# Kernel tuning notes

Hardware: AMD Instinct MI355X
Metric: run time of the kernel (lower is better)

## Reference

```python
import jax, jax.numpy as jnp
import numpy as np

STRIDE = (1, 1)
PADDING = ((1, 1), (1, 1))


def setup_inputs() -> dict:
    key = jax.random.key(0)
    kx, kw, kb = jax.random.split(key, 3)
    x = jax.random.normal(kx, (32, 128, 56, 56), dtype=jnp.float32)
    weight = jax.random.normal(kw, (256, 128, 3, 3), dtype=jnp.float32)  # (O, I, kh, kw)
    bias = jax.random.normal(kb, (256,), dtype=jnp.float32)
    return {"x": x, "weight": weight, "bias": bias}


def reference(x, weight, bias):
    # Faithful dense 2D convolution (cross-correlation, as in the torch module),
    # NCHW input, OIHW weight, stride 1, padding 1.
    out = jax.lax.conv_general_dilated(
        x, weight,
        window_strides=STRIDE,
        padding=PADDING,
        dimension_numbers=("NCHW", "OIHW", "NCHW"),
    )
    return out + bias[None, :, None, None]
```

## Files before the change

kernel.cpp:

```cpp
#include <hip/hip_runtime.h>

#define C_IN   128
#define H_IN   56
#define W_IN   56
#define HW     3136
#define CHW    401408
#define O_OUT  256
#define OHW    802816

#define BM 256
#define BN 128
#define LDSW 64
#define LDK 72
#define XTP 132

typedef __bf16 bf16x8 __attribute__((ext_vector_type(8)));
typedef float  f32x4  __attribute__((ext_vector_type(4)));
typedef unsigned short ushort_t;
typedef ushort_t ushort8 __attribute__((ext_vector_type(8)));

__device__ __forceinline__ ushort_t f2bf(float f) {
    union { float f; unsigned u; } v; v.f = f;
    unsigned r = (v.u + 0x7fffu + ((v.u >> 16) & 1u)) >> 16;
    return (ushort_t)r;
}

__global__ void wt_kernel(const float* __restrict__ w, ushort_t* __restrict__ wbf) {
    int idx = blockIdx.x * 256 + threadIdx.x;
    if (idx >= 9 * 256 * 128) return;
    int pos = idx >> 15;
    int rem = idx & 32767;
    int o   = rem >> 7;
    int c   = rem & 127;
    wbf[idx] = f2bf(w[o * 1152 + c * 9 + pos]);
}

__global__ __launch_bounds__(256)
void xt_kernel(const float* __restrict__ x, ushort_t* __restrict__ xb) {
    __shared__ ushort_t T[64 * XTP];
    const int t  = threadIdx.x;
    const int tb = blockIdx.x;
    const int n   = tb / 49;
    const int hw0 = (tb - n * 49) * 64;
    const float* src = x + (long)n * CHW + hw0;

    #pragma unroll
    for (int i = 0; i < 8; ++i) {
        const int g  = i * 256 + t;
        const int c  = g >> 4;
        const int p4 = g & 15;
        f32x4 v = *(const f32x4*)(src + (long)c * HW + p4 * 4);
        #pragma unroll
        for (int j = 0; j < 4; ++j)
            T[(p4 * 4 + j) * XTP + c] = f2bf(v[j]);
    }
    __syncthreads();

    ushort_t* dst = xb + ((long)n * HW + hw0) * 128;
    #pragma unroll
    for (int s = 0; s < 4; ++s) {
        const int idx = s * 256 + t;
        const int pix = idx >> 4;
        const int grp = idx & 15;
        ushort8 v = *(const ushort8*)(&T[pix * XTP + grp * 8]);
        *(ushort8*)(dst + pix * 128 + grp * 8) = v;
    }
}

__global__ __launch_bounds__(512, 4)
void conv2_kernel(const ushort_t* __restrict__ xb, const ushort_t* __restrict__ wbf,
                  const float* __restrict__ bias, float* __restrict__ out) {
    __shared__ ushort_t As[BM * LDSW];
    __shared__ ushort_t Bs[BN * LDSW];

    const int tid  = threadIdx.x;
    const int lane = tid & 63;
    const int wave = tid >> 6;
    const int wm   = wave >> 1;
    const int wn   = wave & 1;
    const int l15  = lane & 15;
    const int quad = lane >> 4;

    const int pix_base = blockIdx.x * BN;

    const int bpx = tid >> 2;
    const int bg0 = (tid & 3) * 2;
    const int p   = pix_base + bpx;
    const int n_img = p / HW;
    const int hw    = p - n_img * HW;
    const int h     = hw / W_IN;
    const int w_    = hw - h * W_IN;

    const int ao = tid >> 3;
    const int ag = tid & 7;

    f32x4 acc[4][4];
    #pragma unroll
    for (int t = 0; t < 4; ++t)
        #pragma unroll
        for (int u = 0; u < 4; ++u)
            acc[t][u] = f32x4{0.f, 0.f, 0.f, 0.f};

    for (int pos = 0; pos < 9; ++pos) {
        const int dh = pos / 3 - 1;
        const int dw = pos - (pos / 3) * 3 - 1;
        const int ih = h + dh;
        const int iw = w_ + dw;
        const bool valid = ((unsigned)ih < (unsigned)H_IN) && ((unsigned)iw < (unsigned)W_IN);
        const ushort_t* bsrc = xb + (long)(p + dh * W_IN + dw) * 128;

        #pragma unroll
        for (int half = 0; half < 2; ++half) {
            const int c0 = half * 64;

            {
                const ushort_t* wsrc = wbf + pos * 32768 + c0;
                #pragma unroll
                for (int s = 0; s < 4; ++s) {
                    const int o = ao + s * 64;
                    ushort8 v = *(const ushort8*)(wsrc + (o << 7) + ag * 8);
                    *(ushort8*)(&As[o * LDSW + ((ag ^ (o & 7)) * 8)]) = v;
                }
            }
            {
                #pragma unroll
                for (int q = 0; q < 2; ++q) {
                    const int g = bg0 + q;
                    ushort8 v;
                    if (valid) v = *(const ushort8*)(bsrc + c0 + g * 8);
                    else       v = ushort8{0,0,0,0,0,0,0,0};
                    *(ushort8*)(&Bs[bpx * LDSW + ((g ^ (bpx & 7)) * 8)]) = v;
                }
            }
            __syncthreads();

            #pragma unroll
            for (int ks = 0; ks < 2; ++ks) {
                bf16x8 af[4], bfv[4];
                const int k16 = ks * 4 + quad;
                #pragma unroll
                for (int t = 0; t < 4; ++t) {
                    const int row = wm * 64 + t * 16 + l15;
                    af[t] = *(const bf16x8*)(&As[row * LDSW + ((k16 ^ (row & 7)) * 8)]);
                }
                #pragma unroll
                for (int u = 0; u < 4; ++u) {
                    const int col = wn * 64 + u * 16 + l15;
                    bfv[u] = *(const bf16x8*)(&Bs[col * LDSW + ((k16 ^ (col & 7)) * 8)]);
                }
                #pragma unroll
                for (int t = 0; t < 4; ++t)
                    #pragma unroll
                    for (int u = 0; u < 4; ++u)
                        acc[t][u] = __builtin_amdgcn_mfma_f32_16x16x32_bf16(af[t], bfv[u], acc[t][u], 0, 0, 0);
            }
            __syncthreads();
        }
    }

    #pragma unroll
    for (int u = 0; u < 4; ++u) {
        const int col = wn * 64 + u * 16 + l15;
        const int pp  = pix_base + col;
        const int nn  = pp / HW;
        const int hw2 = pp - nn * HW;
        const long obase = (long)nn * OHW + hw2;
        #pragma unroll
        for (int t = 0; t < 4; ++t) {
            const int o_base = wm * 64 + t * 16 + quad * 4;
            #pragma unroll
            for (int r = 0; r < 4; ++r) {
                const int o = o_base + r;
                out[obase + (long)o * HW] = acc[t][u][r] + bias[o];
            }
        }
    }
}

__global__ __launch_bounds__(512, 4)
void conv_kernel(const float* __restrict__ x, const ushort_t* __restrict__ wbf,
                 const float* __restrict__ bias, float* __restrict__ out) {
    __shared__ ushort_t As[BM * LDK];
    __shared__ ushort_t Bs[BN * LDK];

    const int tid  = threadIdx.x;
    const int lane = tid & 63;
    const int wave = tid >> 6;
    const int wm   = wave >> 1;
    const int wn   = wave & 1;
    const int l15  = lane & 15;
    const int quad = lane >> 4;

    const int pix_base = blockIdx.x * BN;
    const int px  = tid & 127;
    const int cg0 = tid >> 7;
    const int p   = pix_base + px;
    const int n_img = p / HW;
    const int hw    = p - n_img * HW;
    const int h     = hw / W_IN;
    const int w_    = hw - h * W_IN;
    const float* ximg = x + (long)n_img * CHW;

    f32x4 acc[4][4];
    #pragma unroll
    for (int t = 0; t < 4; ++t)
        #pragma unroll
        for (int u = 0; u < 4; ++u)
            acc[t][u] = f32x4{0.f, 0.f, 0.f, 0.f};

    for (int pos = 0; pos < 9; ++pos) {
        const int dh = pos / 3 - 1;
        const int dw = pos - (pos / 3) * 3 - 1;
        const int ih = h + dh;
        const int iw = w_ + dw;
        const bool valid = ((unsigned)ih < (unsigned)H_IN) && ((unsigned)iw < (unsigned)W_IN);
        const float* xsrc = ximg + ih * W_IN + iw;

        for (int half = 0; half < 2; ++half) {
            const int c0 = half * 64;
            {
                const ushort_t* wsrc = wbf + ((pos * 256) << 7) + c0;
                #pragma unroll
                for (int s = 0; s < 4; ++s) {
                    const int o  = (tid >> 3) + s * 64;
                    const int cg = tid & 7;
                    ushort8 v = *(const ushort8*)(wsrc + (o << 7) + cg * 8);
                    *(ushort8*)(&As[o * LDK + cg * 8]) = v;
                }
            }
            {
                #pragma unroll
                for (int s = 0; s < 2; ++s) {
                    const int cg = cg0 + s * 4;
                    const float* src = xsrc + (long)(c0 + cg * 8) * HW;
                    ushort8 v;
                    #pragma unroll
                    for (int j = 0; j < 8; ++j) {
                        float f = valid ? src[j * HW] : 0.0f;
                        v[j] = f2bf(f);
                    }
                    *(ushort8*)(&Bs[px * LDK + cg * 8]) = v;
                }
            }
            __syncthreads();

            #pragma unroll
            for (int ks = 0; ks < 2; ++ks) {
                bf16x8 af[4], bfv[4];
                #pragma unroll
                for (int t = 0; t < 4; ++t) {
                    const int row = wm * 64 + t * 16 + l15;
                    af[t] = *(const bf16x8*)(&As[row * LDK + ks * 32 + quad * 8]);
                }
                #pragma unroll
                for (int u = 0; u < 4; ++u) {
                    const int col = wn * 64 + u * 16 + l15;
                    bfv[u] = *(const bf16x8*)(&Bs[col * LDK + ks * 32 + quad * 8]);
                }
                #pragma unroll
                for (int t = 0; t < 4; ++t)
                    #pragma unroll
                    for (int u = 0; u < 4; ++u)
                        acc[t][u] = __builtin_amdgcn_mfma_f32_16x16x32_bf16(af[t], bfv[u], acc[t][u], 0, 0, 0);
            }
            __syncthreads();
        }
    }

    #pragma unroll
    for (int u = 0; u < 4; ++u) {
        const int col = wn * 64 + u * 16 + l15;
        const int pp  = pix_base + col;
        const int hw2 = pp - (pp / HW) * HW;
        const long obase = (long)(pp / HW) * OHW + hw2;
        #pragma unroll
        for (int t = 0; t < 4; ++t) {
            const int o_base = wm * 64 + t * 16 + quad * 4;
            #pragma unroll
            for (int r = 0; r < 4; ++r) {
                const int o = o_base + r;
                out[obase + (long)o * HW] = acc[t][u][r] + bias[o];
            }
        }
    }
}

extern "C" void kernel_launch(void* const* d_in, const int* in_sizes, int n_in,
                              void* d_out, int out_size, void* d_ws, size_t ws_size,
                              hipStream_t stream) {
    const float* x    = (const float*)d_in[0];
    const float* w    = (const float*)d_in[1];
    const float* bias = (const float*)d_in[2];
    float* out        = (float*)d_out;

    ushort_t* wbf = (ushort_t*)d_ws;
    ushort_t* xb  = (ushort_t*)((char*)d_ws + 589824);

    const size_t need = 589824u + 25690112u;

    hipLaunchKernelGGL(wt_kernel, dim3(1152), dim3(256), 0, stream, w, wbf);
    if (ws_size >= need) {
        hipLaunchKernelGGL(xt_kernel, dim3(1568), dim3(256), 0, stream, x, xb);
        hipLaunchKernelGGL(conv2_kernel, dim3(100352 / BN), dim3(512), 0, stream,
                           xb, wbf, bias, out);
    } else {
        hipLaunchKernelGGL(conv_kernel, dim3(100352 / BN), dim3(512), 0, stream,
                           x, wbf, bias, out);
    }
}
```

Before: 226.0 us.

## Add padded-NHWC patch conv kernel with LDS-resident input rows and async weight prefetch

Adds a new path: the input is transposed to a zero-padded, swizzled NHWC bf16 layout, and weights are pre-swizzled per 64-channel slice. Each block loads a 6-row input patch (4 output rows plus halo) into LDS once via global_load_lds and reuses it across all 9 filter taps. Weight slices are double-buffered with asynchronous global-to-LDS loads overlapping the MFMA work. This removes repeated per-tap input fetches and bounds checks, at the cost of a larger workspace, heavy LDS use and a larger per-thread accumulator tile (28 MFMA tiles) that may limit occupancy.

```diff
diff --git a/kernel.cpp b/kernel.cpp
--- a/kernel.cpp
+++ b/kernel.cpp
@@ -14,6 +14,10 @@
 #define LDK 72
 #define XTP 132
 
+#define PH 58
+#define PROW 7424
+#define PATCH_PIX 348
+
 typedef __bf16 bf16x8 __attribute__((ext_vector_type(8)));
 typedef float  f32x4  __attribute__((ext_vector_type(4)));
 typedef unsigned short ushort_t;
@@ -24,6 +28,191 @@
     unsigned r = (v.u + 0x7fffu + ((v.u >> 16) & 1u)) >> 16;
     return (ushort_t)r;
 }
+
+typedef const __attribute__((address_space(1))) unsigned int* gas_ptr;
+typedef __attribute__((address_space(3))) unsigned int* las_ptr;
+__device__ __forceinline__ void gl_lds16(const void* g, void* l) {
+    __builtin_amdgcn_global_load_lds((gas_ptr)g, (las_ptr)l, 16, 0, 0);
+}
+
+
+__global__ void wt2_kernel(const float* __restrict__ w, ushort_t* __restrict__ wbf) {
+    int idx = blockIdx.x * 256 + threadIdx.x;
+    if (idx >= 9 * 256 * 128) return;
+    int pos = idx >> 15;
+    int rem = idx & 32767;
+    int o   = rem >> 7;
+    int c   = rem & 127;
+    int s    = pos * 2 + (c >> 6);
+    int slot = ((c >> 3) & 7) ^ (o & 7);
+    wbf[((s * 256 + o) << 6) + (slot << 3) + (c & 7)] = f2bf(w[o * 1152 + c * 9 + pos]);
+}
+
+__global__ __launch_bounds__(256)
+void xt2_kernel(const float* __restrict__ x, ushort_t* __restrict__ xbp) {
+    const int b  = blockIdx.x;
+    const int n  = b / PH;
+    const int hp = b - n * PH;
+    ushort_t* orow = xbp + (size_t)(n * PH + hp) * PROW;
+    const int t = threadIdx.x;
+    ushort8 z = ushort8{0,0,0,0,0,0,0,0};
+
+    if (hp == 0 || hp == 57) {
+        #pragma unroll
+        for (int i = 0; i < 4; ++i) {
+            int u = i * 256 + t;
+            if (u < 928) *(ushort8*)(orow + u * 8) = z;
+        }
+        return;
+    }
+
+    __shared__ ushort_t T[56 * XTP];
+    const int h = hp - 1;
+    const float* src = x + (size_t)n * CHW + h * W_IN;
+    #pragma unroll
+    for (int i = 0; i < 7; ++i) {
+        int g  = i * 256 + t;
+        int c  = g / 14;
+        int f4 = g - c * 14;
+        f32x4 v = *(const f32x4*)(src + (size_t)c * HW + f4 * 4);
+        #pragma unroll
+        for (int j = 0; j < 4; ++j)
+            T[(f4 * 4 + j) * XTP + c] = f2bf(v[j]);
+    }
+    __syncthreads();
+    #pragma unroll
+    for (int i = 0; i < 4; ++i) {
+        int u = i * 256 + t;
+        if (u < 928) {
+            int wp = u >> 4, gg = u & 15;
+            ushort8 v = (wp == 0 || wp == 57) ? z
+                        : *(const ushort8*)(&T[(wp - 1) * XTP + gg * 8]);
+            *(ushort8*)(orow + wp * 128 + ((gg ^ (wp & 7)) << 3)) = v;
+        }
+    }
+}
+
+__global__ __launch_bounds__(512, 2)
+void conv3_kernel(const ushort_t* __restrict__ xbp, const ushort_t* __restrict__ wbf,
+                  const float* __restrict__ bias, float* __restrict__ out) {
+    __shared__ ushort_t patch[PATCH_PIX * 128];
+    __shared__ ushort_t wlds[2][256 * 64];
+
+    const int tid  = threadIdx.x;
+    const int lane = tid & 63;
+    const int wave = tid >> 6;
+    const int wm   = wave >> 1;
+    const int wn   = wave & 1;
+    const int l15  = lane & 15;
+    const int quad = lane >> 4;
+    const int om   = wm * 64;
+
+    const int b  = blockIdx.x;
+    const int n  = b / 14;
+    const int hg = b - n * 14;
+    const int h0 = hg * 4;
+
+    int ppix[7], wlo[7], obo[7];
+    #pragma unroll
+    for (int u = 0; u < 7; ++u) {
+        int p  = wn * 112 + u * 16 + l15;
+        int pr = p / 56;
+        int ww = p - pr * 56;
+        ppix[u] = (pr * PH + ww) * 128;
+        wlo[u]  = ww;
+        obo[u]  = (h0 + pr) * W_IN + ww;
+    }
+
+    f32x4 acc[4][7];
+    #pragma unroll
+    for (int t = 0; t < 4; ++t)
+        #pragma unroll
+        for (int u = 0; u < 7; ++u)
+            acc[t][u] = f32x4{0.f, 0.f, 0.f, 0.f};
+
+    {
+        const char* xs = (const char*)(xbp + (size_t)(n * PH + h0) * PROW);
+        char* pb = (char*)patch;
+        #pragma unroll
+        for (int jj = 0; jj < 11; ++jj) {
+            int j = jj * 8 + wave;
+            if (j < 87) gl_lds16(xs + j * 1024 + lane * 16, pb + j * 1024);
+        }
+        const char* wg = (const char*)wbf;
+        char* wb = (char*)wlds[0];
+        #pragma unroll
+        for (int j2 = 0; j2 < 4; ++j2) {
+            int j = j2 * 8 + wave;
+            gl_lds16(wg + j * 1024 + lane * 16, wb + j * 1024);
+        }
+    }
+    asm volatile("s_waitcnt vmcnt(0)" ::: "memory");
+    __syncthreads();
+
+    int s = 0, cur = 0;
+    for (int kh = 0; kh < 3; ++kh) {
+        #pragma unroll
+        for (int kw = 0; kw < 3; ++kw) {
+            const int poff = (kh * PH + kw) * 128;
+            #pragma unroll
+            for (int half = 0; half < 2; ++half) {
+                const ushort_t* wcur = wlds[cur];
+                if (s < 17) {
+                    const char* wg = (const char*)wbf + (size_t)(s + 1) * 32768;
+                    char* wb = (char*)wlds[cur ^ 1];
+                    #pragma unroll
+                    for (int j2 = 0; j2 < 4; ++j2) {
+                        int j = j2 * 8 + wave;
+                        gl_lds16(wg + j * 1024 + lane * 16, wb + j * 1024);
+                    }
+                }
+                #pragma unroll
+                for (int ks = 0; ks < 2; ++ks) {
+                    const int k8  = ks * 4 + quad;
+                    const int k16 = half * 8 + k8;
+                    bf16x8 af[4], bfv[7];
+                    #pragma unroll
+                    for (int t = 0; t < 4; ++t) {
+                        int o = om + t * 16 + l15;
+                        af[t] = *(const bf16x8*)(wcur + (o << 6) + ((k8 ^ (o & 7)) << 3));
+                    }
+                    #pragma unroll
+                    for (int u = 0; u < 7; ++u) {
+                        int slot = k16 ^ ((wlo[u] + kw) & 7);
+                        bfv[u] = *(const bf16x8*)(patch + ppix[u] + poff + (slot << 3));
+                    }
+                    #pragma unroll
+                    for (int t = 0; t < 4; ++t)
+                        #pragma unroll
+                        for (int u = 0; u < 7; ++u)
+                            acc[t][u] = __builtin_amdgcn_mfma_f32_16x16x32_bf16(
+                                            af[t], bfv[u], acc[t][u], 0, 0, 0);
+                }
+                asm volatile("s_waitcnt vmcnt(0)" ::: "memory");
+                __syncthreads();
+                cur ^= 1; ++s;
+            }
+        }
+    }
+
+    f32x4 bv[4];
+    #pragma unroll
+    for (int t = 0; t < 4; ++t)
+        bv[t] = *(const f32x4*)(bias + om + t * 16 + quad * 4);
+    float* outn = out + (size_t)n * OHW;
+    #pragma unroll
+    for (int u = 0; u < 7; ++u) {
+        float* op = outn + obo[u];
+        #pragma unroll
+        for (int t = 0; t < 4; ++t) {
+            const int o0 = om + t * 16 + quad * 4;
+            #pragma unroll
+            for (int r = 0; r < 4; ++r)
+                op[(size_t)(o0 + r) * HW] = acc[t][u][r] + bv[t][r];
+        }
+    }
+}
+
 
 __global__ void wt_kernel(const float* __restrict__ w, ushort_t* __restrict__ wbf) {
     int idx = blockIdx.x * 256 + threadIdx.x;
@@ -116,8 +305,8 @@
             {
                 const ushort_t* wsrc = wbf + pos * 32768 + c0;
                 #pragma unroll
-                for (int s = 0; s < 4; ++s) {
-                    const int o = ao + s * 64;
+                for (int sj = 0; sj < 4; ++sj) {
+                    const int o = ao + sj * 64;
                     ushort8 v = *(const ushort8*)(wsrc + (o << 7) + ag * 8);
                     *(ushort8*)(&As[o * LDSW + ((ag ^ (o & 7)) * 8)]) = v;
                 }
@@ -221,8 +410,8 @@
             {
                 const ushort_t* wsrc = wbf + ((pos * 256) << 7) + c0;
                 #pragma unroll
-                for (int s = 0; s < 4; ++s) {
-                    const int o  = (tid >> 3) + s * 64;
+                for (int sj = 0; sj < 4; ++sj) {
+                    const int o  = (tid >> 3) + sj * 64;
                     const int cg = tid & 7;
                     ushort8 v = *(const ushort8*)(wsrc + (o << 7) + cg * 8);
                     *(ushort8*)(&As[o * LDK + cg * 8]) = v;
@@ -230,8 +419,8 @@
             }
             {
                 #pragma unroll
-                for (int s = 0; s < 2; ++s) {
-                    const int cg = cg0 + s * 4;
+                for (int sj = 0; sj < 2; ++sj) {
+                    const int cg = cg0 + sj * 4;
                     const float* src = xsrc + (long)(c0 + cg * 8) * HW;
                     ushort8 v;
                     #pragma unroll
@@ -293,17 +482,26 @@
     const float* bias = (const float*)d_in[2];
     float* out        = (float*)d_out;
 
-    ushort_t* wbf = (ushort_t*)d_ws;
-    ushort_t* xb  = (ushort_t*)((char*)d_ws + 589824);
-
-    const size_t need = 589824u + 25690112u;
-
-    hipLaunchKernelGGL(wt_kernel, dim3(1152), dim3(256), 0, stream, w, wbf);
-    if (ws_size >= need) {
+    const size_t NEED_NEW = 589824u + 27557888u;
+    const size_t NEED_OLD = 589824u + 25690112u;
+
+    if (ws_size >= NEED_NEW) {
+        ushort_t* wbf2 = (ushort_t*)d_ws;
+        ushort_t* xbp  = (ushort_t*)((char*)d_ws + 589824);
+        hipLaunchKernelGGL(wt2_kernel, dim3(1152), dim3(256), 0, stream, w, wbf2);
+        hipLaunchKernelGGL(xt2_kernel, dim3(1856), dim3(256), 0, stream, x, xbp);
+        hipLaunchKernelGGL(conv3_kernel, dim3(448), dim3(512), 0, stream,
+                           xbp, wbf2, bias, out);
+    } else if (ws_size >= NEED_OLD) {
+        ushort_t* wbf = (ushort_t*)d_ws;
+        ushort_t* xb  = (ushort_t*)((char*)d_ws + 589824);
+        hipLaunchKernelGGL(wt_kernel, dim3(1152), dim3(256), 0, stream, w, wbf);
         hipLaunchKernelGGL(xt_kernel, dim3(1568), dim3(256), 0, stream, x, xb);
         hipLaunchKernelGGL(conv2_kernel, dim3(100352 / BN), dim3(512), 0, stream,
                            xb, wbf, bias, out);
     } else {
+        ushort_t* wbf = (ushort_t*)d_ws;
+        hipLaunchKernelGGL(wt_kernel, dim3(1152), dim3(256), 0, stream, w, wbf);
         hipLaunchKernelGGL(conv_kernel, dim3(100352 / BN), dim3(512), 0, stream,
                            x, wbf, bias, out);
     }
```

Result: slower. 237.7 us (+5.2%).

## Replace im2col GEMM with halo-patch conv kernel reading weights from global

Applied to the files above, without the earlier changes.

The separate NHWC bf16 transpose pass and the per-tap LDS staging are replaced by a kernel where each block loads a 4x58x128 bf16 halo patch of input once into swizzled LDS. All nine taps then reuse it for two output rows (112 pixels) across 256 output channels. Weights are rearranged into per-tap, per-half slabs and read directly from global/L2 into registers, with no LDS or barriers in the main loop. This removes the extra transpose kernel and repeated input traffic, but relies on L2 for weight bandwidth. It also adds a serial, strided fp32 patch load done by only 232 threads at block start.

```diff
diff --git a/kernel.cpp b/kernel.cpp
--- a/kernel.cpp
+++ b/kernel.cpp
@@ -8,11 +8,7 @@
 #define O_OUT  256
 #define OHW    802816
 
-#define BM 256
-#define BN 128
-#define LDSW 64
 #define LDK 72
-#define XTP 132
 
 typedef __bf16 bf16x8 __attribute__((ext_vector_type(8)));
 typedef float  f32x4  __attribute__((ext_vector_type(4)));
@@ -24,6 +20,130 @@
     unsigned r = (v.u + 0x7fffu + ((v.u >> 16) & 1u)) >> 16;
     return (ushort_t)r;
 }
+
+__global__ void wt3_kernel(const float* __restrict__ w, ushort_t* __restrict__ wbf) {
+    int idx = blockIdx.x * 256 + threadIdx.x;
+    if (idx >= 9 * 256 * 128) return;
+    int pos = idx >> 15;
+    int rem = idx & 32767;
+    int o   = rem >> 7;
+    int c   = rem & 127;
+    int s   = pos * 2 + (c >> 6);
+    wbf[((s * 256 + o) << 6) + (c & 63)] = f2bf(w[o * 1152 + c * 9 + pos]);
+}
+
+__global__ __launch_bounds__(256, 2)
+void conv6_kernel(const float* __restrict__ x, const ushort_t* __restrict__ wbf,
+                  const float* __restrict__ bias, float* __restrict__ out) {
+    __shared__ ushort_t patch[232 * 128];
+
+    const int tid  = threadIdx.x;
+    const int lane = tid & 63;
+    const int wave = tid >> 6;
+    const int l15  = lane & 15;
+    const int quad = lane >> 4;
+    const int om   = wave * 64;
+
+    int b = blockIdx.x;
+    b = (b & 7) * 112 + (b >> 3);
+    const int n  = b / 28;
+    const int h0 = (b - n * 28) * 2;
+
+    if (tid < 232) {
+        const int pr = tid / 58;
+        const int wp = tid - pr * 58;
+        const int ih = h0 - 1 + pr;
+        const int iw = wp - 1;
+        const bool ok = ((unsigned)ih < 56u) && ((unsigned)iw < 56u);
+        const float* xs = x + (size_t)n * CHW + ih * W_IN + iw;
+        ushort_t* dst = patch + tid * 128;
+        const int wkey = wp & 7;
+        #pragma unroll
+        for (int cg = 0; cg < 16; ++cg) {
+            ushort8 v;
+            #pragma unroll
+            for (int j = 0; j < 8; ++j) {
+                float f = 0.0f;
+                if (ok) f = xs[(size_t)(cg * 8 + j) * HW];
+                v[j] = f2bf(f);
+            }
+            *(ushort8*)(dst + (((cg ^ wkey)) << 3)) = v;
+        }
+    }
+    __syncthreads();
+
+    int ppix[7], wk[7], obo[7];
+    #pragma unroll
+    for (int u = 0; u < 7; ++u) {
+        int pix = u * 16 + l15;
+        int pr  = (pix >= 56) ? 1 : 0;
+        int ww  = pix - pr * 56;
+        ppix[u] = (pr * 58 + ww) * 128;
+        wk[u]   = ww;
+        obo[u]  = (h0 + pr) * W_IN + ww;
+    }
+
+    int aoff[4];
+    #pragma unroll
+    for (int t = 0; t < 4; ++t)
+        aoff[t] = ((om + t * 16 + l15) << 6) + (quad << 3);
+
+    f32x4 acc[4][7];
+    #pragma unroll
+    for (int t = 0; t < 4; ++t)
+        #pragma unroll
+        for (int u = 0; u < 7; ++u)
+            acc[t][u] = f32x4{0.f, 0.f, 0.f, 0.f};
+
+    for (int kh = 0; kh < 3; ++kh) {
+        #pragma unroll
+        for (int kw = 0; kw < 3; ++kw) {
+            const int poff = (kh * 58 + kw) * 128;
+            #pragma unroll
+            for (int half = 0; half < 2; ++half) {
+                const int s = (kh * 3 + kw) * 2 + half;
+                const ushort_t* wsp = wbf + (size_t)s * 16384;
+                #pragma unroll
+                for (int ks = 0; ks < 2; ++ks) {
+                    bf16x8 af[4], bfv[7];
+                    #pragma unroll
+                    for (int t = 0; t < 4; ++t)
+                        af[t] = *(const bf16x8*)(wsp + aoff[t] + ks * 32);
+                    const int k16 = half * 8 + ks * 4 + quad;
+                    #pragma unroll
+                    for (int u = 0; u < 7; ++u) {
+                        const int slot = k16 ^ ((wk[u] + kw) & 7);
+                        bfv[u] = *(const bf16x8*)(patch + ppix[u] + poff + (slot << 3));
+                    }
+                    #pragma unroll
+                    for (int t = 0; t < 4; ++t)
+                        #pragma unroll
+                        for (int u = 0; u < 7; ++u)
+                            acc[t][u] = __builtin_amdgcn_mfma_f32_16x16x32_bf16(
+                                            af[t], bfv[u], acc[t][u], 0, 0, 0);
+                }
+            }
+        }
+    }
+
+    f32x4 bv[4];
+    #pragma unroll
+    for (int t = 0; t < 4; ++t)
+        bv[t] = *(const f32x4*)(bias + om + t * 16 + quad * 4);
+    float* outn = out + (size_t)n * OHW;
+    #pragma unroll
+    for (int u = 0; u < 7; ++u) {
+        float* op = outn + obo[u];
+        #pragma unroll
+        for (int t = 0; t < 4; ++t) {
+            const int o0 = om + t * 16 + quad * 4;
+            #pragma unroll
+            for (int r = 0; r < 4; ++r)
+                op[(size_t)(o0 + r) * HW] = acc[t][u][r] + bv[t][r];
+        }
+    }
+}
+
 
 __global__ void wt_kernel(const float* __restrict__ w, ushort_t* __restrict__ wbf) {
     int idx = blockIdx.x * 256 + threadIdx.x;
@@ -35,43 +155,11 @@
     wbf[idx] = f2bf(w[o * 1152 + c * 9 + pos]);
 }
 
-__global__ __launch_bounds__(256)
-void xt_kernel(const float* __restrict__ x, ushort_t* __restrict__ xb) {
-    __shared__ ushort_t T[64 * XTP];
-    const int t  = threadIdx.x;
-    const int tb = blockIdx.x;
-    const int n   = tb / 49;
-    const int hw0 = (tb - n * 49) * 64;
-    const float* src = x + (long)n * CHW + hw0;
-
-    #pragma unroll
-    for (int i = 0; i < 8; ++i) {
-        const int g  = i * 256 + t;
-        const int c  = g >> 4;
-        const int p4 = g & 15;
-        f32x4 v = *(const f32x4*)(src + (long)c * HW + p4 * 4);
-        #pragma unroll
-        for (int j = 0; j < 4; ++j)
-            T[(p4 * 4 + j) * XTP + c] = f2bf(v[j]);
-    }
-    __syncthreads();
-
-    ushort_t* dst = xb + ((long)n * HW + hw0) * 128;
-    #pragma unroll
-    for (int s = 0; s < 4; ++s) {
-        const int idx = s * 256 + t;
-        const int pix = idx >> 4;
-        const int grp = idx & 15;
-        ushort8 v = *(const ushort8*)(&T[pix * XTP + grp * 8]);
-        *(ushort8*)(dst + pix * 128 + grp * 8) = v;
-    }
-}
-
 __global__ __launch_bounds__(512, 4)
-void conv2_kernel(const ushort_t* __restrict__ xb, const ushort_t* __restrict__ wbf,
-                  const float* __restrict__ bias, float* __restrict__ out) {
-    __shared__ ushort_t As[BM * LDSW];
-    __shared__ ushort_t Bs[BN * LDSW];
+void conv_kernel(const float* __restrict__ x, const ushort_t* __restrict__ wbf,
+                 const float* __restrict__ bias, float* __restrict__ out) {
+    __shared__ ushort_t As[256 * LDK];
+    __shared__ ushort_t Bs[128 * LDK];
 
     const int tid  = threadIdx.x;
     const int lane = tid & 63;
@@ -81,117 +169,7 @@
     const int l15  = lane & 15;
     const int quad = lane >> 4;
 
-    const int pix_base = blockIdx.x * BN;
-
-    const int bpx = tid >> 2;
-    const int bg0 = (tid & 3) * 2;
-    const int p   = pix_base + bpx;
-    const int n_img = p / HW;
-    const int hw    = p - n_img * HW;
-    const int h     = hw / W_IN;
-    const int w_    = hw - h * W_IN;
-
-    const int ao = tid >> 3;
-    const int ag = tid & 7;
-
-    f32x4 acc[4][4];
-    #pragma unroll
-    for (int t = 0; t < 4; ++t)
-        #pragma unroll
-        for (int u = 0; u < 4; ++u)
-            acc[t][u] = f32x4{0.f, 0.f, 0.f, 0.f};
-
-    for (int pos = 0; pos < 9; ++pos) {
-        const int dh = pos / 3 - 1;
-        const int dw = pos - (pos / 3) * 3 - 1;
-        const int ih = h + dh;
-        const int iw = w_ + dw;
-        const bool valid = ((unsigned)ih < (unsigned)H_IN) && ((unsigned)iw < (unsigned)W_IN);
-        const ushort_t* bsrc = xb + (long)(p + dh * W_IN + dw) * 128;
-
-        #pragma unroll
-        for (int half = 0; half < 2; ++half) {
-            const int c0 = half * 64;
-
-            {
-                const ushort_t* wsrc = wbf + pos * 32768 + c0;
-                #pragma unroll
-                for (int s = 0; s < 4; ++s) {
-                    const int o = ao + s * 64;
-                    ushort8 v = *(const ushort8*)(wsrc + (o << 7) + ag * 8);
-                    *(ushort8*)(&As[o * LDSW + ((ag ^ (o & 7)) * 8)]) = v;
-                }
-            }
-            {
-                #pragma unroll
-                for (int q = 0; q < 2; ++q) {
-                    const int g = bg0 + q;
-                    ushort8 v;
-                    if (valid) v = *(const ushort8*)(bsrc + c0 + g * 8);
-                    else       v = ushort8{0,0,0,0,0,0,0,0};
-                    *(ushort8*)(&Bs[bpx * LDSW + ((g ^ (bpx & 7)) * 8)]) = v;
-                }
-            }
-            __syncthreads();
-
-            #pragma unroll
-            for (int ks = 0; ks < 2; ++ks) {
-                bf16x8 af[4], bfv[4];
-                const int k16 = ks * 4 + quad;
-                #pragma unroll
-                for (int t = 0; t < 4; ++t) {
-                    const int row = wm * 64 + t * 16 + l15;
-                    af[t] = *(const bf16x8*)(&As[row * LDSW + ((k16 ^ (row & 7)) * 8)]);
-                }
-                #pragma unroll
-                for (int u = 0; u < 4; ++u) {
-                    const int col = wn * 64 + u * 16 + l15;
-                    bfv[u] = *(const bf16x8*)(&Bs[col * LDSW + ((k16 ^ (col & 7)) * 8)]);
-                }
-                #pragma unroll
-                for (int t = 0; t < 4; ++t)
-                    #pragma unroll
-                    for (int u = 0; u < 4; ++u)
-                        acc[t][u] = __builtin_amdgcn_mfma_f32_16x16x32_bf16(af[t], bfv[u], acc[t][u], 0, 0, 0);
-            }
-            __syncthreads();
-        }
-    }
-
-    #pragma unroll
-    for (int u = 0; u < 4; ++u) {
-        const int col = wn * 64 + u * 16 + l15;
-        const int pp  = pix_base + col;
-        const int nn  = pp / HW;
-        const int hw2 = pp - nn * HW;
-        const long obase = (long)nn * OHW + hw2;
-        #pragma unroll
-        for (int t = 0; t < 4; ++t) {
-            const int o_base = wm * 64 + t * 16 + quad * 4;
-            #pragma unroll
-            for (int r = 0; r < 4; ++r) {
-                const int o = o_base + r;
-                out[obase + (long)o * HW] = acc[t][u][r] + bias[o];
-            }
-        }
-    }
-}
-
-__global__ __launch_bounds__(512, 4)
-void conv_kernel(const float* __restrict__ x, const ushort_t* __restrict__ wbf,
-                 const float* __restrict__ bias, float* __restrict__ out) {
-    __shared__ ushort_t As[BM * LDK];
-    __shared__ ushort_t Bs[BN * LDK];
-
-    const int tid  = threadIdx.x;
-    const int lane = tid & 63;
-    const int wave = tid >> 6;
-    const int wm   = wave >> 1;
-    const int wn   = wave & 1;
-    const int l15  = lane & 15;
-    const int quad = lane >> 4;
-
-    const int pix_base = blockIdx.x * BN;
+    const int pix_base = blockIdx.x * 128;
     const int px  = tid & 127;
     const int cg0 = tid >> 7;
     const int p   = pix_base + px;
@@ -221,8 +199,8 @@
             {
                 const ushort_t* wsrc = wbf + ((pos * 256) << 7) + c0;
                 #pragma unroll
-                for (int s = 0; s < 4; ++s) {
-                    const int o  = (tid >> 3) + s * 64;
+                for (int sj = 0; sj < 4; ++sj) {
+                    const int o  = (tid >> 3) + sj * 64;
                     const int cg = tid & 7;
                     ushort8 v = *(const ushort8*)(wsrc + (o << 7) + cg * 8);
                     *(ushort8*)(&As[o * LDK + cg * 8]) = v;
@@ -230,8 +208,8 @@
             }
             {
                 #pragma unroll
-                for (int s = 0; s < 2; ++s) {
-                    const int cg = cg0 + s * 4;
+                for (int sj = 0; sj < 2; ++sj) {
+                    const int cg = cg0 + sj * 4;
                     const float* src = xsrc + (long)(c0 + cg * 8) * HW;
                     ushort8 v;
                     #pragma unroll
@@ -294,17 +272,14 @@
     float* out        = (float*)d_out;
 
     ushort_t* wbf = (ushort_t*)d_ws;
-    ushort_t* xb  = (ushort_t*)((char*)d_ws + 589824);
-
-    const size_t need = 589824u + 25690112u;
-
-    hipLaunchKernelGGL(wt_kernel, dim3(1152), dim3(256), 0, stream, w, wbf);
-    if (ws_size >= need) {
-        hipLaunchKernelGGL(xt_kernel, dim3(1568), dim3(256), 0, stream, x, xb);
-        hipLaunchKernelGGL(conv2_kernel, dim3(100352 / BN), dim3(512), 0, stream,
-                           xb, wbf, bias, out);
+
+    if (ws_size >= 589824u) {
+        hipLaunchKernelGGL(wt3_kernel, dim3(1152), dim3(256), 0, stream, w, wbf);
+        hipLaunchKernelGGL(conv6_kernel, dim3(896), dim3(256), 0, stream,
+                           x, wbf, bias, out);
     } else {
-        hipLaunchKernelGGL(conv_kernel, dim3(100352 / BN), dim3(512), 0, stream,
+        hipLaunchKernelGGL(wt_kernel, dim3(1152), dim3(256), 0, stream, w, wbf);
+        hipLaunchKernelGGL(conv_kernel, dim3(100352 / 128), dim3(512), 0, stream,
                            x, wbf, bias, out);
     }
 }
```

After: 226.9 us. About the same (+0.4%).
